# Kernel tuning notes

Hardware: AMD Instinct MI355X
Metric: run time of the kernel (lower is better)

The kernel has to match this reference:

```python
import jax, jax.numpy as jnp
import numpy as np

K = 3
C = 256
C4 = C // 4


def adaptive_avg_pool(x, k):
    # Faithful torch AdaptiveAvgPool2d: bin i covers [floor(i*H/k), ceil((i+1)*H/k))
    N, Ch, H, W = x.shape
    rows = []
    for i in range(k):
        sh, eh = (i * H) // k, -((-(i + 1) * H) // k)
        cols = []
        for j in range(k):
            sw, ew = (j * W) // k, -((-(j + 1) * W) // k)
            cols.append(x[:, :, sh:eh, sw:ew].mean(axis=(2, 3)))
        rows.append(jnp.stack(cols, axis=-1))  # [N,Ch,k]
    return jnp.stack(rows, axis=-2)  # [N,Ch,k,k]


def setup_inputs() -> dict:
    key = jax.random.key(0)
    ks = jax.random.split(key, 6)
    x = jax.random.normal(ks[0], (16, C, 128, 128), dtype=jnp.float32)
    # 1x1 convs stored as dense matrices (spatial 1x1 squeezed)
    conv_w = jax.random.normal(ks[1], (C4, C), dtype=jnp.float32) * (1.0 / np.sqrt(C))
    conv_b = jax.random.normal(ks[2], (C4,), dtype=jnp.float32) * 0.02
    dw_b = jax.random.normal(ks[3], (C4,), dtype=jnp.float32) * 0.02
    fuse_w = jax.random.normal(ks[4], (C, C4), dtype=jnp.float32) * (1.0 / np.sqrt(C4))
    fuse_b = jax.random.normal(ks[5], (C,), dtype=jnp.float32) * 0.02
    return {"x": x, "conv_w": conv_w, "conv_b": conv_b, "dw_b": dw_b,
            "fuse_w": fuse_w, "fuse_b": fuse_b}


def reference(x, conv_w, conv_b, dw_b, fuse_w, fuse_b):
    N, Ch, H, W = x.shape
    k = K
    c4 = conv_w.shape[0]
    # f = conv(x)  (1x1)
    f = jnp.einsum('nchw,oc->nohw', x, conv_w) + conv_b[None, :, None, None]
    # g = conv(pool(x)) -> per-sample depthwise filters [N, C4, k, k]
    xp = adaptive_avg_pool(x, k)
    g = jnp.einsum('nchw,oc->nohw', xp, conv_w) + conv_b[None, :, None, None]
    # batched dynamic depthwise conv: fold batch into groups, one fused conv
    p = (k - 1) // 2
    lhs = f.reshape(1, N * c4, H, W)
    rhs = g.reshape(N * c4, 1, k, k)
    y = jax.lax.conv_general_dilated(
        lhs, rhs, window_strides=(1, 1), padding=[(p, p), (p, p)],
        feature_group_count=N * c4,
        dimension_numbers=('NCHW', 'OIHW', 'NCHW'))
    y = y.reshape(N, c4, H, W) + dw_b[None, :, None, None]
    # fuse (1x1)
    out = jnp.einsum('nchw,oc->nohw', y, fuse_w) + fuse_b[None, :, None, None]
    return out
```

## Files before the change

### kernel.cpp

```cpp
#include <hip/hip_runtime.h>
#include <hip/hip_bf16.h>

#define NB 16
#define C 256
#define C4 64
#define HDIM 128
#define WDIM 128
#define HW 16384

typedef __bf16 bf16x8 __attribute__((ext_vector_type(8)));
typedef float f32x4 __attribute__((ext_vector_type(4)));

__device__ __forceinline__ unsigned short f2bf(float x) {
    union { __bf16 h; unsigned short u; } c;
    c.h = (__bf16)x;
    return c.u;
}
__device__ __forceinline__ float bf2f(unsigned short b) {
    union { float f; unsigned u; } a; a.u = ((unsigned)b) << 16; return a.f;
}

__global__ __launch_bounds__(256) void k0_pack(
    const float* __restrict__ conv_w, const float* __restrict__ fuse_w,
    const float* __restrict__ fuse_b, const float* __restrict__ dw_b,
    unsigned short* __restrict__ cwpk, unsigned short* __restrict__ fwpk,
    float* __restrict__ fbe)
{
    int tid = blockIdx.x * 256 + threadIdx.x;
    {
        int m = tid >> 8, k = tid & 255;
        int frag = (m >> 4) * 8 + (k >> 5);
        int lane = (m & 15) | (((k >> 3) & 3) << 4);
        int e = k & 7;
        cwpk[(frag * 64 + lane) * 8 + e] = f2bf(conv_w[m * 256 + k]);
    }
    {
        int m = tid >> 6, k = tid & 63;
        int frag = (m >> 4) * 2 + (k >> 5);
        int lane = (m & 15) | (((k >> 3) & 3) << 4);
        int e = k & 7;
        fwpk[(frag * 64 + lane) * 8 + e] = f2bf(fuse_w[m * 64 + k]);
    }
    if (tid < 256) {
        float s = fuse_b[tid];
        #pragma unroll
        for (int o = 0; o < 64; ++o) s += fuse_w[tid * 64 + o] * dw_b[o];
        fbe[tid] = s;
    }
}

__global__ __launch_bounds__(256) void k1_conv(
    const float* __restrict__ x, const unsigned short* __restrict__ cwpk,
    const float* __restrict__ conv_b, unsigned short* __restrict__ f_ws,
    float* __restrict__ psum)
{
    __shared__ unsigned short xlds[32 * 138];
    int blk = blockIdx.x;
    int n = blk >> 7;
    int h = blk & 127;
    int p0 = h * WDIM;
    int t = threadIdx.x;
    int lane = t & 63, wv = t >> 6, gq = lane >> 4, l15 = lane & 15;
    const float* xn = x + (size_t)n * C * HW + p0;

    int lch = t >> 5;
    int lpx = (t & 31) * 4;

    f32x4 r[4];
    #pragma unroll
    for (int j = 0; j < 4; ++j)
        r[j] = __builtin_nontemporal_load(
            reinterpret_cast<const f32x4*>(&xn[(size_t)(j * 8 + lch) * HW + lpx]));

    f32x4 acc[2][4];
    #pragma unroll
    for (int pt = 0; pt < 2; ++pt)
        #pragma unroll
        for (int m = 0; m < 4; ++m) acc[pt][m] = (f32x4){0.f, 0.f, 0.f, 0.f};

    for (int kc = 0; kc < 8; ++kc) {
        unsigned int pk[4][2];
        #pragma unroll
        for (int j = 0; j < 4; ++j) {
            pk[j][0] = ((unsigned)f2bf(r[j].y) << 16) | f2bf(r[j].x);
            pk[j][1] = ((unsigned)f2bf(r[j].w) << 16) | f2bf(r[j].z);
        }
        __syncthreads();
        #pragma unroll
        for (int j = 0; j < 4; ++j) {
            unsigned int* dst = reinterpret_cast<unsigned int*>(
                &xlds[(j * 8 + lch) * 138 + lpx]);
            dst[0] = pk[j][0];
            dst[1] = pk[j][1];
        }
        __syncthreads();
        if (kc < 7) {
            #pragma unroll
            for (int j = 0; j < 4; ++j)
                r[j] = __builtin_nontemporal_load(
                    reinterpret_cast<const f32x4*>(
                        &xn[(size_t)((kc + 1) * 32 + j * 8 + lch) * HW + lpx]));
        }
        bf16x8 a[4];
        #pragma unroll
        for (int m = 0; m < 4; ++m)
            a[m] = *reinterpret_cast<const bf16x8*>(cwpk + ((m * 8 + kc) * 64 + lane) * 8);
        #pragma unroll
        for (int pt = 0; pt < 2; ++pt) {
            int px = wv * 32 + pt * 16 + l15;
            union { bf16x8 v; unsigned short u[8]; } b;
            #pragma unroll
            for (int e = 0; e < 8; ++e)
                b.u[e] = xlds[(gq * 8 + e) * 138 + px];
            #pragma unroll
            for (int m = 0; m < 4; ++m)
                acc[pt][m] = __builtin_amdgcn_mfma_f32_16x16x32_bf16(b.v, a[m], acc[pt][m], 0, 0, 0);
        }
    }

    float cbv[4];
    #pragma unroll
    for (int m = 0; m < 4; ++m) cbv[m] = conv_b[m * 16 + l15];

    float cs[4][3];
    #pragma unroll
    for (int m = 0; m < 4; ++m) cs[m][0] = cs[m][1] = cs[m][2] = 0.f;

    unsigned short* fn = f_ws + (size_t)n * C4 * HW;
    #pragma unroll
    for (int pt = 0; pt < 2; ++pt) {
        int pxb = wv * 32 + pt * 16 + gq * 4;
        #pragma unroll
        for (int m = 0; m < 4; ++m) {
            int o = m * 16 + l15;
            union { unsigned int d[2]; unsigned short u[4]; } pk2;
            #pragma unroll
            for (int e = 0; e < 4; ++e) {
                float v = acc[pt][m][e] + cbv[m];
                pk2.u[e] = f2bf(v);
                int px = pxb + e;
                if (px < 43)              cs[m][0] += v;
                if (px >= 42 && px < 86)  cs[m][1] += v;
                if (px >= 85)             cs[m][2] += v;
            }
            *reinterpret_cast<uint2*>(&fn[(size_t)o * HW + p0 + pxb]) =
                (uint2){pk2.d[0], pk2.d[1]};
        }
    }

    #pragma unroll
    for (int m = 0; m < 4; ++m)
        #pragma unroll
        for (int b = 0; b < 3; ++b) {
            float v = cs[m][b];
            v += __shfl_xor(v, 16, 64);
            v += __shfl_xor(v, 32, 64);
            cs[m][b] = v;
        }

    if (gq == 0) {
        float* ps = psum + ((size_t)blk * 4 + wv) * 192;
        #pragma unroll
        for (int m = 0; m < 4; ++m)
            #pragma unroll
            for (int b = 0; b < 3; ++b)
                ps[(m * 16 + l15) * 3 + b] = cs[m][b];
    }
}

__global__ __launch_bounds__(192) void k2_reduce(
    const float* __restrict__ psum, float* __restrict__ gsum)
{
    int n = blockIdx.x;
    int t = threadIdx.x;
    int o = t / 3, cb = t - 3 * o;
    const float* ps = psum + (size_t)n * 128 * 768 + t;
    float s0 = 0.f, s1 = 0.f, s2 = 0.f;
    for (int h = 0; h < 128; ++h) {
        float v = 0.f;
        #pragma unroll
        for (int wv = 0; wv < 4; ++wv) v += ps[h * 768 + wv * 192];
        if (h < 43)            s0 += v;
        if (h >= 42 && h < 86) s1 += v;
        if (h >= 85)           s2 += v;
    }
    float* gp = gsum + (n * 64 + o) * 9;
    gp[0 + cb] = s0;
    gp[3 + cb] = s1;
    gp[6 + cb] = s2;
}

__global__ __launch_bounds__(512) void k3_dwfuse(
    const unsigned short* __restrict__ f_ws, const float* __restrict__ gsum,
    const unsigned short* __restrict__ fwpk, const float* __restrict__ fbe,
    float* __restrict__ out)
{
    __shared__ unsigned short ylds[64][136];
    int blk = blockIdx.x;
    int n = blk >> 7;
    int h = blk & 127;
    int t = threadIdx.x;

    {
        const float ginv[9] = {
            1.f/1849.f, 1.f/1892.f, 1.f/1849.f,
            1.f/1892.f, 1.f/1936.f, 1.f/1892.f,
            1.f/1849.f, 1.f/1892.f, 1.f/1849.f };
        int o = t >> 3, q = t & 7;
        int wb = q * 16;
        const unsigned short* fp = f_ws + (size_t)(n * 64 + o) * HW;
        const float* gp = gsum + (n * 64 + o) * 9;
        float gv[9];
        #pragma unroll
        for (int k = 0; k < 9; ++k) gv[k] = gp[k] * ginv[k];
        float y[16];
        #pragma unroll
        for (int i = 0; i < 16; ++i) y[i] = 0.f;
        #pragma unroll
        for (int dy = -1; dy <= 1; ++dy) {
            int hh = h + dy;
            if (hh < 0 || hh >= HDIM) continue;
            const unsigned short* row = fp + hh * WDIM;
            union { uint4 q4; unsigned short u[8]; } bA, bB;
            bA.q4 = *reinterpret_cast<const uint4*>(row + wb);
            bB.q4 = *reinterpret_cast<const uint4*>(row + wb + 8);
            float lft = bf2f(row[wb == 0 ? 0 : wb - 1]);
            if (wb == 0)   lft = 0.f;
            float rgt = bf2f(row[wb == 112 ? 127 : wb + 16]);
            if (wb == 112) rgt = 0.f;
            float rv[18];
            rv[0] = lft;
            #pragma unroll
            for (int z = 0; z < 8; ++z) rv[1 + z] = bf2f(bA.u[z]);
            #pragma unroll
            for (int z = 0; z < 8; ++z) rv[9 + z] = bf2f(bB.u[z]);
            rv[17] = rgt;
            float g0 = gv[(dy + 1) * 3], g1 = gv[(dy + 1) * 3 + 1], g2 = gv[(dy + 1) * 3 + 2];
            #pragma unroll
            for (int i = 0; i < 16; ++i)
                y[i] += g0 * rv[i] + g1 * rv[i + 1] + g2 * rv[i + 2];
        }
        union { uint4 q4[2]; unsigned short u[16]; } pk;
        #pragma unroll
        for (int i = 0; i < 16; ++i) pk.u[i] = f2bf(y[i]);
        *reinterpret_cast<uint4*>(&ylds[o][wb])     = pk.q4[0];
        *reinterpret_cast<uint4*>(&ylds[o][wb + 8]) = pk.q4[1];
    }
    __syncthreads();

    int lane = t & 63, wv = t >> 6, gq = lane >> 4, l15 = lane & 15;
    int chb = (wv & 3) * 64, pxb = (wv >> 2) * 64;
    f32x4 acc[4][4];
    #pragma unroll
    for (int a = 0; a < 4; ++a)
        #pragma unroll
        for (int b = 0; b < 4; ++b) acc[a][b] = (f32x4){0.f,0.f,0.f,0.f};

    #pragma unroll
    for (int kc = 0; kc < 2; ++kc) {
        bf16x8 bfr[4];
        #pragma unroll
        for (int pj = 0; pj < 4; ++pj) {
            union { bf16x8 v; unsigned short u[8]; } bb;
            #pragma unroll
            for (int e = 0; e < 8; ++e)
                bb.u[e] = ylds[kc * 32 + gq * 8 + e][pxb + pj * 16 + l15];
            bfr[pj] = bb.v;
        }
        #pragma unroll
        for (int mc = 0; mc < 4; ++mc) {
            int mtile = (wv & 3) * 4 + mc;
            bf16x8 a = *reinterpret_cast<const bf16x8*>(
                fwpk + ((mtile * 2 + kc) * 64 + lane) * 8);
            #pragma unroll
            for (int pj = 0; pj < 4; ++pj)
                acc[mc][pj] = __builtin_amdgcn_mfma_f32_16x16x32_bf16(bfr[pj], a, acc[mc][pj], 0, 0, 0);
        }
    }

    size_t outbase = (size_t)n * C * HW + (size_t)h * WDIM;
    #pragma unroll
    for (int mc = 0; mc < 4; ++mc) {
        int c = chb + mc * 16 + l15;
        float bias = fbe[c];
        #pragma unroll
        for (int pj = 0; pj < 4; ++pj) {
            int w = pxb + pj * 16 + gq * 4;
            f32x4 vv;
            #pragma unroll
            for (int e = 0; e < 4; ++e) vv[e] = acc[mc][pj][e] + bias;
            *reinterpret_cast<f32x4*>(&out[outbase + (size_t)c * HW + w]) = vv;
        }
    }
}

extern "C" void kernel_launch(void* const* d_in, const int* in_sizes, int n_in,
                              void* d_out, int out_size, void* d_ws, size_t ws_size,
                              hipStream_t stream) {
    const float* x      = (const float*)d_in[0];
    const float* conv_w = (const float*)d_in[1];
    const float* conv_b = (const float*)d_in[2];
    const float* dw_b   = (const float*)d_in[3];
    const float* fuse_w = (const float*)d_in[4];
    const float* fuse_b = (const float*)d_in[5];
    float* out = (float*)d_out;

    char* ws = (char*)d_ws;
    unsigned short* f_ws = (unsigned short*)ws;
    float* psum          = (float*)(ws + 33554432);
    float* gsum          = (float*)(ws + 33554432 + 6291456);
    unsigned short* cwpk = (unsigned short*)(ws + 33554432 + 6291456 + 36864);
    unsigned short* fwpk = (unsigned short*)(ws + 33554432 + 6291456 + 36864 + 32768);
    float* fbe           = (float*)(ws + 33554432 + 6291456 + 36864 + 32768 + 32768);

    k0_pack<<<dim3(64), dim3(256), 0, stream>>>(conv_w, fuse_w, fuse_b, dw_b, cwpk, fwpk, fbe);
    k1_conv<<<dim3(2048), dim3(256), 0, stream>>>(x, cwpk, conv_b, f_ws, psum);
    k2_reduce<<<dim3(16), dim3(192), 0, stream>>>(psum, gsum);
    k3_dwfuse<<<dim3(2048), dim3(512), 0, stream>>>(f_ws, gsum, fwpk, fbe, out);
}
```

Before: 151.0 us.

## Pre-reduce wave partial sums in LDS and parallelize pooled-sum reduction

The conv kernel now sums its four per-wave pooling partials through shared memory before writing, so it emits one 192-float record per block instead of four. The reduction kernel goes from 16 blocks that loop serially over 128 rows to 1024 blocks, each reducing one (sample, channel) pair across rows with wave shuffles. This removes a long serial tail on a mostly idle GPU and cuts partial-sum traffic, at the cost of an extra __syncthreads in the conv kernel.

```diff
diff --git a/kernel.cpp b/kernel.cpp
--- a/kernel.cpp
+++ b/kernel.cpp
@@ -55,6 +55,7 @@
     float* __restrict__ psum)
 {
     __shared__ unsigned short xlds[32 * 138];
+    __shared__ float xpool[4][192];
     int blk = blockIdx.x;
     int n = blk >> 7;
     int h = blk & 127;
@@ -159,35 +160,49 @@
         }
 
     if (gq == 0) {
-        float* ps = psum + ((size_t)blk * 4 + wv) * 192;
         #pragma unroll
         for (int m = 0; m < 4; ++m)
             #pragma unroll
             for (int b = 0; b < 3; ++b)
-                ps[(m * 16 + l15) * 3 + b] = cs[m][b];
-    }
-}
-
-__global__ __launch_bounds__(192) void k2_reduce(
+                xpool[wv][(m * 16 + l15) * 3 + b] = cs[m][b];
+    }
+    __syncthreads();
+    if (t < 192)
+        psum[(size_t)blk * 192 + t] =
+            xpool[0][t] + xpool[1][t] + xpool[2][t] + xpool[3][t];
+}
+
+__global__ __launch_bounds__(128) void k2_reduce(
     const float* __restrict__ psum, float* __restrict__ gsum)
 {
-    int n = blockIdx.x;
-    int t = threadIdx.x;
-    int o = t / 3, cb = t - 3 * o;
-    const float* ps = psum + (size_t)n * 128 * 768 + t;
-    float s0 = 0.f, s1 = 0.f, s2 = 0.f;
-    for (int h = 0; h < 128; ++h) {
-        float v = 0.f;
-        #pragma unroll
-        for (int wv = 0; wv < 4; ++wv) v += ps[h * 768 + wv * 192];
-        if (h < 43)            s0 += v;
-        if (h >= 42 && h < 86) s1 += v;
-        if (h >= 85)           s2 += v;
-    }
-    float* gp = gsum + (n * 64 + o) * 9;
-    gp[0 + cb] = s0;
-    gp[3 + cb] = s1;
-    gp[6 + cb] = s2;
+    int bid = blockIdx.x;
+    int n = bid >> 6, o = bid & 63;
+    int h = threadIdx.x;
+    const float* ps = psum + ((size_t)(n * 128 + h)) * 192 + o * 3;
+    float v0 = ps[0], v1 = ps[1], v2 = ps[2];
+
+    float s[9];
+    #pragma unroll
+    for (int k = 0; k < 9; ++k) s[k] = 0.f;
+    if (h < 43)            { s[0] += v0; s[1] += v1; s[2] += v2; }
+    if (h >= 42 && h < 86) { s[3] += v0; s[4] += v1; s[5] += v2; }
+    if (h >= 85)           { s[6] += v0; s[7] += v1; s[8] += v2; }
+
+    int lane = h & 63, wid = h >> 6;
+    #pragma unroll
+    for (int k = 0; k < 9; ++k) {
+        float v = s[k];
+        for (int off = 32; off > 0; off >>= 1) v += __shfl_down(v, off, 64);
+        s[k] = v;
+    }
+    __shared__ float red[2][9];
+    if (lane == 0) {
+        #pragma unroll
+        for (int k = 0; k < 9; ++k) red[wid][k] = s[k];
+    }
+    __syncthreads();
+    if (threadIdx.x < 9)
+        gsum[(n * 64 + o) * 9 + threadIdx.x] = red[0][threadIdx.x] + red[1][threadIdx.x];
 }
 
 __global__ __launch_bounds__(512) void k3_dwfuse(
@@ -308,13 +323,13 @@
     char* ws = (char*)d_ws;
     unsigned short* f_ws = (unsigned short*)ws;
     float* psum          = (float*)(ws + 33554432);
-    float* gsum          = (float*)(ws + 33554432 + 6291456);
-    unsigned short* cwpk = (unsigned short*)(ws + 33554432 + 6291456 + 36864);
-    unsigned short* fwpk = (unsigned short*)(ws + 33554432 + 6291456 + 36864 + 32768);
-    float* fbe           = (float*)(ws + 33554432 + 6291456 + 36864 + 32768 + 32768);
+    float* gsum          = (float*)(ws + 33554432 + 2097152);
+    unsigned short* cwpk = (unsigned short*)(ws + 33554432 + 2097152 + 36864);
+    unsigned short* fwpk = (unsigned short*)(ws + 33554432 + 2097152 + 36864 + 32768);
+    float* fbe           = (float*)(ws + 33554432 + 2097152 + 36864 + 32768 + 32768);
 
     k0_pack<<<dim3(64), dim3(256), 0, stream>>>(conv_w, fuse_w, fuse_b, dw_b, cwpk, fwpk, fbe);
     k1_conv<<<dim3(2048), dim3(256), 0, stream>>>(x, cwpk, conv_b, f_ws, psum);
-    k2_reduce<<<dim3(16), dim3(192), 0, stream>>>(psum, gsum);
+    k2_reduce<<<dim3(1024), dim3(128), 0, stream>>>(psum, gsum);
     k3_dwfuse<<<dim3(2048), dim3(512), 0, stream>>>(f_ws, gsum, fwpk, fbe, out);
 }
```

Result: faster. 138.2 us (-8.5%).
